# Performance work log

Measured on AMD Instinct MI355X. Metric: run time of the kernel, lower is better.

The kernel has to match this reference:

```python
import jax, jax.numpy as jnp
import numpy as np

H = 128  # hidden size
I = 5    # input size


def setup_inputs() -> dict:
    key = jax.random.key(0)
    ks = jax.random.split(key, 8)
    B, T = 2048, 512
    s_ih = 1.0 / np.sqrt(H)
    x = jax.random.normal(ks[0], (B, T, I), dtype=jnp.float32)
    # PyTorch LSTM params, gate order (i, f, g, o)
    W_ih = jax.random.uniform(ks[1], (4 * H, I), jnp.float32, -s_ih, s_ih)
    W_hh = jax.random.uniform(ks[2], (4 * H, H), jnp.float32, -s_ih, s_ih)
    b_ih = jax.random.uniform(ks[3], (4 * H,), jnp.float32, -s_ih, s_ih)
    b_hh = jax.random.uniform(ks[4], (4 * H,), jnp.float32, -s_ih, s_ih)
    W_lin = jax.random.uniform(ks[5], (1, H), jnp.float32, -s_ih, s_ih)
    b_lin = jax.random.uniform(ks[6], (1,), jnp.float32, -s_ih, s_ih)
    return {"x": x, "W_ih": W_ih, "W_hh": W_hh, "b_ih": b_ih,
            "b_hh": b_hh, "W_lin": W_lin, "b_lin": b_lin}


def _lstm_final_h(x, W_ih, W_hh, b_ih, b_hh):
    B = x.shape[0]
    # Precompute input projection for all timesteps: [B, T, 4H]
    x_proj = jnp.einsum('bti,gi->btg', x, W_ih) + b_ih + b_hh

    def step(carry, xt):
        h, c = carry
        gates = xt + h @ W_hh.T  # [B, 4H]
        i, f, g, o = jnp.split(gates, 4, axis=-1)
        i = jax.nn.sigmoid(i)
        f = jax.nn.sigmoid(f)
        g = jnp.tanh(g)
        o = jax.nn.sigmoid(o)
        c = f * c + i * g
        h = o * jnp.tanh(c)
        return (h, c), None

    h0 = jnp.zeros((B, H), dtype=x.dtype)
    c0 = jnp.zeros((B, H), dtype=x.dtype)
    (h_n, _), _ = jax.lax.scan(step, (h0, c0), jnp.swapaxes(x_proj, 0, 1))
    return h_n  # [B, H]


def reference(x, W_ih, W_hh, b_ih, b_hh, W_lin, b_lin):
    h_n = _lstm_final_h(x, W_ih, W_hh, b_ih, b_hh)
    # h_n.reshape(num_layers*B, H) @ linear -> [B, 1]
    return h_n @ W_lin.T + b_lin
```

## Files before the change

kernel.cpp:

```cpp
#include <hip/hip_runtime.h>


#define HH 128
#define II 5
#define TT 512
#define BT 8
#define NT 512
#define KS 136
#define XT (TT * 8 + 8)
#define HB (16 * KS)

typedef __attribute__((ext_vector_type(8))) _Float16 half8;
typedef __attribute__((ext_vector_type(4))) _Float16 half4;
typedef __attribute__((ext_vector_type(4))) float f32x4;

#define SIG(u) __builtin_amdgcn_rcpf(1.0f + __builtin_amdgcn_exp2f(u))
#define MF32(A, B, C) __builtin_amdgcn_mfma_f32_16x16x32_f16((A), (B), (C), 0, 0, 0)
#define MF16(A, B, C) __builtin_amdgcn_mfma_f32_16x16x16f16((A), (B), (C), 0, 0, 0)
#define SGB(m, n) __builtin_amdgcn_sched_group_barrier((m), (n), 0)

#define STEP(PB, LAST) {                                                        \
    const _Float16* hp = hrd + (PB) * HB;                                       \
    ah0 = *reinterpret_cast<const half8*>(hp);                                  \
    ah1 = *reinterpret_cast<const half8*>(hp + 32);                             \
    ah2 = *reinterpret_cast<const half8*>(hp + 64);                             \
    ah3 = *reinterpret_cast<const half8*>(hp + 96);                             \
                                                           \
    f32x4 a0 = MF16(ax4, wfx[0], zero4);                                        \
    f32x4 a1 = MF16(ax4, wfx[1], zero4);                                        \
    a0 = MF32(ah0, wf[0][0], a0); a1 = MF32(ah0, wf[1][0], a1);                 \
    a0 = MF32(ah1, wf[0][1], a0); a1 = MF32(ah1, wf[1][1], a1);                 \
    a0 = MF32(ah2, wf[0][2], a0); a1 = MF32(ah2, wf[1][2], a1);                 \
    a0 = MF32(ah3, wf[0][3], a0); a1 = MF32(ah3, wf[1][3], a1);                 \
         \
    float iv0 = SIG(a0[0]);                                                     \
    float iv1 = SIG(a0[1]);                                                     \
    float fv0 = SIG(a1[0]);                                                     \
    float fv1 = SIG(a1[1]);                                                     \
    f32x4 a2 = MF16(ax4, wfx[2], zero4);                                        \
    f32x4 a3 = MF16(ax4, wfx[3], zero4);                                        \
    a2 = MF32(ah0, wf[2][0], a2); a3 = MF32(ah0, wf[3][0], a3);                 \
    a2 = MF32(ah1, wf[2][1], a2); a3 = MF32(ah1, wf[3][1], a3);                 \
    a2 = MF32(ah2, wf[2][2], a2); a3 = MF32(ah2, wf[3][2], a3);                 \
    a2 = MF32(ah3, wf[2][3], a2); a3 = MF32(ah3, wf[3][3], a3);                 \
    if (!(LAST)) {                             \
        xcur += xinc;                                                           \
        ax4 = *reinterpret_cast<const half4*>(xcur);                            \
    }                                                                           \
    float gv0 = 1.0f - 2.0f * SIG(a2[0]);                                       \
    float ov0 = SIG(a3[0]);                                                     \
    cc0 = fv0 * cc0 + iv0 * gv0;                                                \
    float hv0 = ov0 * (1.0f - 2.0f * SIG(2.88539008f * cc0));                   \
    float gv1 = 1.0f - 2.0f * SIG(a2[1]);                                       \
    float ov1 = SIG(a3[1]);                                                     \
    cc1 = fv1 * cc1 + iv1 * gv1;                                                \
    float hv1 = ov1 * (1.0f - 2.0f * SIG(2.88539008f * cc1));                   \
    if (LAST) {                                                                 \
        hsc[bcell][hcol] = hv0; hsc[bcell + 1][hcol] = hv1;                     \
    } else {                                                                    \
        _Float16* wp = hwr + ((PB) ^ 1) * HB;                                   \
        wp[0]  = (_Float16)hv0;                                                 \
        wp[KS] = (_Float16)hv1;                                                 \
    }                                                                           \
    \
    SGB(0x100, 4);                                    \
    SGB(0x008, 10);                                        \
    SGB(0x402, 14);         \
    SGB(0x008, 10);                                        \
    __syncthreads();                                                            \
}

__global__ __launch_bounds__(NT)
__attribute__((amdgpu_waves_per_eu(2, 2)))
void lstm_r12(const float* __restrict__ x,
              const float* __restrict__ W_ih,
              const float* __restrict__ W_hh,
              const float* __restrict__ b_ih,
              const float* __restrict__ b_hh,
              const float* __restrict__ W_lin,
              const float* __restrict__ b_lin,
              float* __restrict__ out,
              int B)
{
    __shared__ __align__(16) _Float16 hbuf[2][16][KS];
    __shared__ __align__(16) _Float16 zrow[KS];
    __shared__ __align__(16) _Float16 xs[BT * XT];
    __shared__ float hsc[BT][HH + 4];

    const int tid  = threadIdx.x;
    const int b0   = blockIdx.x * BT;
    const int lane = tid & 63;
    const int w    = tid >> 6;
    const int n    = lane & 15;
    const int q    = lane >> 4;
    const int q8   = q * 8;
    const int hcol = w * 16 + n;

    half8 wf[4][4];
    half4 wfx[4];
    #pragma unroll
    for (int g = 0; g < 4; ++g) {
        const float sc = (g == 2) ? 2.88539008f : -1.44269504f;
        const int j = g * HH + hcol;
        #pragma unroll
        for (int kc = 0; kc < 4; ++kc) {
            const float* p = W_hh + (size_t)j * HH + kc * 32 + q8;
            #pragma unroll
            for (int e = 0; e < 8; ++e) wf[g][kc][e] = (_Float16)(p[e] * sc);
        }
        #pragma unroll
        for (int e = 0; e < 4; ++e) {
            const int k = q * 4 + e;
            float v = 0.0f;
            if (k < II)       v = W_ih[j * II + k];
            else if (k == II) v = b_ih[j] + b_hh[j];
            wfx[g][e] = (_Float16)(v * sc);
        }
    }

    for (int idx = tid; idx < 2 * 16 * KS; idx += NT)
        (&hbuf[0][0][0])[idx] = (_Float16)0.0f;
    if (tid < KS) zrow[tid] = (_Float16)0.0f;
    for (int idx = tid; idx < BT * XT; idx += NT)
        xs[idx] = (_Float16)0.0f;
    __syncthreads();

    {
        const int lb = tid & 63, bb = tid >> 6;
        if (b0 + bb < B) {
            const float* xb = x + (size_t)(b0 + bb) * TT * II;
            for (int e = lb * 4; e < TT * II; e += 256) {
                float4 v = *reinterpret_cast<const float4*>(xb + e);
                float vv[4] = {v.x, v.y, v.z, v.w};
                #pragma unroll
                for (int u = 0; u < 4; ++u) {
                    const int ee = e + u;
                    xs[bb * XT + (ee / 5) * 8 + (ee % 5)] = (_Float16)vv[u];
                }
            }
        }
        for (int s = tid; s < BT * TT; s += NT)
            xs[(s >> 9) * XT + (s & 511) * 8 + 5] = (_Float16)1.0f;
    }
    __syncthreads();

    const int bcell = 2 * q;
    float cc0 = 0.f, cc1 = 0.f;
    const f32x4 zero4 = {0.f, 0.f, 0.f, 0.f};
    const bool xreal = ((n & 2) == 0);
    const int  bofn  = (n >> 2) * 2 + (n & 1);
    const _Float16* hrd  = &hbuf[0][n][0] + q8;
    _Float16*       hwr  = &hbuf[0][q * 4][0] + hcol;
    const _Float16* xcur = xreal ? (&xs[bofn * XT] + q * 4) : (&zrow[0] + q * 4);
    const int       xinc = xreal ? 8 : 0;

    half8 ah0, ah1, ah2, ah3;
    half4 ax4 = *reinterpret_cast<const half4*>(xcur);

    #pragma unroll 1
    for (int k = 0; k < (TT - 2) / 2; ++k) {
        STEP(0, false);
        STEP(1, false);
    }
    STEP(0, false);
    STEP(1, true);

    float p = hsc[w][lane] * W_lin[lane] + hsc[w][lane + 64] * W_lin[lane + 64];
    #pragma unroll
    for (int off = 32; off > 0; off >>= 1) p += __shfl_down(p, off, 64);
    if (lane == 0 && (b0 + w) < B) out[b0 + w] = p + b_lin[0];
}

extern "C" void kernel_launch(void* const* d_in, const int* in_sizes, int n_in,
                              void* d_out, int out_size, void* d_ws, size_t ws_size,
                              hipStream_t stream) {
    const float* x     = (const float*)d_in[0];
    const float* W_ih  = (const float*)d_in[1];
    const float* W_hh  = (const float*)d_in[2];
    const float* b_ih  = (const float*)d_in[3];
    const float* b_hh  = (const float*)d_in[4];
    const float* W_lin = (const float*)d_in[5];
    const float* b_lin = (const float*)d_in[6];
    float* out = (float*)d_out;

    const int B = in_sizes[0] / (TT * II);
    const int grid = (B + BT - 1) / BT;
    lstm_r12<<<grid, NT, 0, stream>>>(x, W_ih, W_hh, b_ih, b_hh,
                                      W_lin, b_lin, out, B);
}
```

Baseline: 343.8 us.

## Quantize recurrent weights and hidden state to int8 and use int8 MFMA

New measurement: 325.7 us. -5.3%, faster.

```diff
diff --git a/kernel.cpp b/kernel.cpp
--- a/kernel.cpp
+++ b/kernel.cpp
@@ -6,73 +6,67 @@
 #define TT 512
 #define BT 8
 #define NT 512
+#define K8S 144
+#define HB8 (16 * K8S)
 #define KS 136
 #define XT (TT * 8 + 8)
-#define HB (16 * KS)
 
-typedef __attribute__((ext_vector_type(8))) _Float16 half8;
 typedef __attribute__((ext_vector_type(4))) _Float16 half4;
 typedef __attribute__((ext_vector_type(4))) float f32x4;
+typedef __attribute__((ext_vector_type(4))) int int4v;
 
 #define SIG(u) __builtin_amdgcn_rcpf(1.0f + __builtin_amdgcn_exp2f(u))
-#define MF32(A, B, C) __builtin_amdgcn_mfma_f32_16x16x32_f16((A), (B), (C), 0, 0, 0)
 #define MF16(A, B, C) __builtin_amdgcn_mfma_f32_16x16x16f16((A), (B), (C), 0, 0, 0)
-#define SGB(m, n) __builtin_amdgcn_sched_group_barrier((m), (n), 0)
+#define MI8(A, B, C)  __builtin_amdgcn_mfma_i32_16x16x64_i8((A), (B), (C), 0, 0, 0)
+
+#define INV_IFO (-1.44269504f / 130048.0f)
+#define INV_G   ( 2.88539008f / 130048.0f)
 
 #define STEP(PB, LAST) {                                                        \
-    const _Float16* hp = hrd + (PB) * HB;                                       \
-    ah0 = *reinterpret_cast<const half8*>(hp);                                  \
-    ah1 = *reinterpret_cast<const half8*>(hp + 32);                             \
-    ah2 = *reinterpret_cast<const half8*>(hp + 64);                             \
-    ah3 = *reinterpret_cast<const half8*>(hp + 96);                             \
-                                                           \
-    f32x4 a0 = MF16(ax4, wfx[0], zero4);                                        \
-    f32x4 a1 = MF16(ax4, wfx[1], zero4);                                        \
-    a0 = MF32(ah0, wf[0][0], a0); a1 = MF32(ah0, wf[1][0], a1);                 \
-    a0 = MF32(ah1, wf[0][1], a0); a1 = MF32(ah1, wf[1][1], a1);                 \
-    a0 = MF32(ah2, wf[0][2], a0); a1 = MF32(ah2, wf[1][2], a1);                 \
-    a0 = MF32(ah3, wf[0][3], a0); a1 = MF32(ah3, wf[1][3], a1);                 \
-         \
-    float iv0 = SIG(a0[0]);                                                     \
-    float iv1 = SIG(a0[1]);                                                     \
-    float fv0 = SIG(a1[0]);                                                     \
-    float fv1 = SIG(a1[1]);                                                     \
-    f32x4 a2 = MF16(ax4, wfx[2], zero4);                                        \
-    f32x4 a3 = MF16(ax4, wfx[3], zero4);                                        \
-    a2 = MF32(ah0, wf[2][0], a2); a3 = MF32(ah0, wf[3][0], a3);                 \
-    a2 = MF32(ah1, wf[2][1], a2); a3 = MF32(ah1, wf[3][1], a3);                 \
-    a2 = MF32(ah2, wf[2][2], a2); a3 = MF32(ah2, wf[3][2], a3);                 \
-    a2 = MF32(ah3, wf[2][3], a2); a3 = MF32(ah3, wf[3][3], a3);                 \
+    const unsigned char* hp = hrd8 + (PB) * HB8;                                \
+    int4v alo = *reinterpret_cast<const int4v*>(hp);                            \
+    int4v ahi = *reinterpret_cast<const int4v*>(hp + 64);                       \
+           \
+    f32x4 xp0 = MF16(ax4, wfx[0], zero4);                                       \
+    f32x4 xp1 = MF16(ax4, wfx[1], zero4);                                       \
+    f32x4 xp2 = MF16(ax4, wfx[2], zero4);                                       \
+    f32x4 xp3 = MF16(ax4, wfx[3], zero4);                                       \
+                                        \
+    int4v s0 = MI8(alo, wq[0][0], zeroi); int4v s1 = MI8(alo, wq[1][0], zeroi); \
+    s0 = MI8(ahi, wq[0][1], s0);          s1 = MI8(ahi, wq[1][1], s1);          \
+          \
+    float iv0 = SIG(fmaf((float)s0[0], INV_IFO, xp0[0]));                       \
+    float iv1 = SIG(fmaf((float)s0[1], INV_IFO, xp0[1]));                       \
+    float fv0 = SIG(fmaf((float)s1[0], INV_IFO, xp1[0]));                       \
+    float fv1 = SIG(fmaf((float)s1[1], INV_IFO, xp1[1]));                       \
+                                                             \
+    int4v s2 = MI8(alo, wq[2][0], zeroi); int4v s3 = MI8(alo, wq[3][0], zeroi); \
+    s2 = MI8(ahi, wq[2][1], s2);          s3 = MI8(ahi, wq[3][1], s3);          \
     if (!(LAST)) {                             \
         xcur += xinc;                                                           \
         ax4 = *reinterpret_cast<const half4*>(xcur);                            \
     }                                                                           \
-    float gv0 = 1.0f - 2.0f * SIG(a2[0]);                                       \
-    float ov0 = SIG(a3[0]);                                                     \
+    float gv0 = 1.0f - 2.0f * SIG(fmaf((float)s2[0], INV_G, xp2[0]));           \
+    float ov0 = SIG(fmaf((float)s3[0], INV_IFO, xp3[0]));                       \
     cc0 = fv0 * cc0 + iv0 * gv0;                                                \
     float hv0 = ov0 * (1.0f - 2.0f * SIG(2.88539008f * cc0));                   \
-    float gv1 = 1.0f - 2.0f * SIG(a2[1]);                                       \
-    float ov1 = SIG(a3[1]);                                                     \
+    float gv1 = 1.0f - 2.0f * SIG(fmaf((float)s2[1], INV_G, xp2[1]));           \
+    float ov1 = SIG(fmaf((float)s3[1], INV_IFO, xp3[1]));                       \
     cc1 = fv1 * cc1 + iv1 * gv1;                                                \
     float hv1 = ov1 * (1.0f - 2.0f * SIG(2.88539008f * cc1));                   \
     if (LAST) {                                                                 \
         hsc[bcell][hcol] = hv0; hsc[bcell + 1][hcol] = hv1;                     \
     } else {                                                                    \
-        _Float16* wp = hwr + ((PB) ^ 1) * HB;                                   \
-        wp[0]  = (_Float16)hv0;                                                 \
-        wp[KS] = (_Float16)hv1;                                                 \
+        unsigned char* wp = hwr8 + ((PB) ^ 1) * HB8;                            \
+        wp[0]    = (unsigned char)(signed char)(int)rintf(hv0 * 127.0f);        \
+        wp[K8S]  = (unsigned char)(signed char)(int)rintf(hv1 * 127.0f);        \
     }                                                                           \
-    \
-    SGB(0x100, 4);                                    \
-    SGB(0x008, 10);                                        \
-    SGB(0x402, 14);         \
-    SGB(0x008, 10);                                        \
     __syncthreads();                                                            \
 }
 
 __global__ __launch_bounds__(NT)
 __attribute__((amdgpu_waves_per_eu(2, 2)))
-void lstm_r12(const float* __restrict__ x,
+void lstm_r17(const float* __restrict__ x,
               const float* __restrict__ W_ih,
               const float* __restrict__ W_hh,
               const float* __restrict__ b_ih,
@@ -82,7 +76,7 @@
               float* __restrict__ out,
               int B)
 {
-    __shared__ __align__(16) _Float16 hbuf[2][16][KS];
+    __shared__ __align__(16) unsigned char hb8[2][16][K8S];
     __shared__ __align__(16) _Float16 zrow[KS];
     __shared__ __align__(16) _Float16 xs[BT * XT];
     __shared__ float hsc[BT][HH + 4];
@@ -93,20 +87,27 @@
     const int w    = tid >> 6;
     const int n    = lane & 15;
     const int q    = lane >> 4;
-    const int q8   = q * 8;
     const int hcol = w * 16 + n;
 
-    half8 wf[4][4];
+    int4v wq[4][2];
     half4 wfx[4];
     #pragma unroll
     for (int g = 0; g < 4; ++g) {
         const float sc = (g == 2) ? 2.88539008f : -1.44269504f;
         const int j = g * HH + hcol;
         #pragma unroll
-        for (int kc = 0; kc < 4; ++kc) {
-            const float* p = W_hh + (size_t)j * HH + kc * 32 + q8;
+        for (int half = 0; half < 2; ++half) {
+            const float* p = W_hh + (size_t)j * HH + half * 64 + q * 16;
             #pragma unroll
-            for (int e = 0; e < 8; ++e) wf[g][kc][e] = (_Float16)(p[e] * sc);
+            for (int r = 0; r < 4; ++r) {
+                int wd = 0;
+                #pragma unroll
+                for (int u = 0; u < 4; ++u) {
+                    int b = (int)rintf(p[r * 4 + u] * 1024.0f);
+                    wd |= (b & 0xff) << (8 * u);
+                }
+                wq[g][half][r] = wd;
+            }
         }
         #pragma unroll
         for (int e = 0; e < 4; ++e) {
@@ -118,8 +119,8 @@
         }
     }
 
-    for (int idx = tid; idx < 2 * 16 * KS; idx += NT)
-        (&hbuf[0][0][0])[idx] = (_Float16)0.0f;
+    for (int idx = tid; idx < 2 * 16 * K8S; idx += NT)
+        (&hb8[0][0][0])[idx] = 0;
     if (tid < KS) zrow[tid] = (_Float16)0.0f;
     for (int idx = tid; idx < BT * XT; idx += NT)
         xs[idx] = (_Float16)0.0f;
@@ -147,14 +148,14 @@
     const int bcell = 2 * q;
     float cc0 = 0.f, cc1 = 0.f;
     const f32x4 zero4 = {0.f, 0.f, 0.f, 0.f};
+    const int4v zeroi = {0, 0, 0, 0};
     const bool xreal = ((n & 2) == 0);
     const int  bofn  = (n >> 2) * 2 + (n & 1);
-    const _Float16* hrd  = &hbuf[0][n][0] + q8;
-    _Float16*       hwr  = &hbuf[0][q * 4][0] + hcol;
+    const unsigned char* hrd8 = &hb8[0][n][0] + q * 16;
+    unsigned char*       hwr8 = &hb8[0][q * 4][0] + hcol;
     const _Float16* xcur = xreal ? (&xs[bofn * XT] + q * 4) : (&zrow[0] + q * 4);
     const int       xinc = xreal ? 8 : 0;
 
-    half8 ah0, ah1, ah2, ah3;
     half4 ax4 = *reinterpret_cast<const half4*>(xcur);
 
     #pragma unroll 1
@@ -185,6 +186,6 @@
 
     const int B = in_sizes[0] / (TT * II);
     const int grid = (B + BT - 1) / BT;
-    lstm_r12<<<grid, NT, 0, stream>>>(x, W_ih, W_hh, b_ih, b_hh,
+    lstm_r17<<<grid, NT, 0, stream>>>(x, W_ih, W_hh, b_ih, b_hh,
                                       W_lin, b_lin, out, B);
 }
```
